# Kernel optimization log

Measured on AMD Instinct MI355X. Metric: run time of the kernel, lower is better.

Reference implementation:

```python
import jax, jax.numpy as jnp
import numpy as np

EPS = 1e-6

def layernorm2d(x, w, b):
    # x: [B,C,H,W]; normalize over channel dim per spatial location
    mu = jnp.mean(x, axis=1, keepdims=True)
    var = jnp.var(x, axis=1, keepdims=True)
    xn = (x - mu) / jnp.sqrt(var + EPS)
    return xn * w[None, :, None, None] + b[None, :, None, None]

def mish(x):
    return x * jnp.tanh(jax.nn.softplus(x))

def setup_inputs() -> dict:
    key = jax.random.key(0)
    ks = jax.random.split(key, 16)
    B, C, H, W, T = 16, 192, 96, 96, 512
    s = 0.02
    return {
        "t": jax.random.normal(ks[0], (B, T), jnp.float32),
        "x_l": jax.random.normal(ks[1], (B, C, H, W), jnp.float32),
        "x_r": jax.random.normal(ks[2], (B, C, H, W), jnp.float32),
        "ln_wl": jnp.ones((C,), jnp.float32),
        "ln_bl": jnp.zeros((C,), jnp.float32),
        "ln_wr": jnp.ones((C,), jnp.float32),
        "ln_br": jnp.zeros((C,), jnp.float32),
        "Wl1": jax.random.normal(ks[3], (C, C), jnp.float32) * s,
        "bl1": jnp.zeros((C,), jnp.float32),
        "Wr1": jax.random.normal(ks[4], (C, C), jnp.float32) * s,
        "br1": jnp.zeros((C,), jnp.float32),
        "Wl2": jax.random.normal(ks[5], (C, C), jnp.float32) * s,
        "bl2": jnp.zeros((C,), jnp.float32),
        "Wr2": jax.random.normal(ks[6], (C, C), jnp.float32) * s,
        "br2": jnp.zeros((C,), jnp.float32),
        "beta": jnp.zeros((C,), jnp.float32),
        "gamma": jnp.zeros((C,), jnp.float32),
        "Wt": jax.random.normal(ks[7], (C, T), jnp.float32) * s,
        "bt": jnp.zeros((C,), jnp.float32),
    }

def reference(t, x_l, x_r, ln_wl, ln_bl, ln_wr, ln_br,
              Wl1, bl1, Wr1, br1, Wl2, bl2, Wr2, br2,
              beta, gamma, Wt, bt):
    C = x_l.shape[1]
    scale = C ** (-0.5)
    # 1x1 convs as channel einsums; outputs in bhwc layout
    Q_l = jnp.einsum('bchw,oc->bhwo', layernorm2d(x_l, ln_wl, ln_bl), Wl1) + bl1  # [B,H,Wl,C]
    Q_r = jnp.einsum('bchw,oc->bhwo', layernorm2d(x_r, ln_wr, ln_br), Wr1) + br1  # [B,H,Wr,C]
    V_l = jnp.einsum('bchw,oc->bhwo', x_l, Wl2) + bl2
    V_r = jnp.einsum('bchw,oc->bhwo', x_r, Wr2) + br2
    att = jnp.einsum('bhxc,bhyc->bhxy', Q_l, Q_r) * scale  # [B,H,Wl,Wr]
    F_r2l = jnp.einsum('bhxy,bhyc->bhxc', jax.nn.softmax(att, axis=-1), V_r)
    F_l2r = jnp.einsum('bhxy,bhxc->bhyc', jax.nn.softmax(att, axis=2), V_l)
    temb = (mish(t) @ Wt.T + bt)[:, :, None, None]  # [B,C,1,1]
    out_l = x_l + jnp.transpose(F_r2l, (0, 3, 1, 2)) * beta[None, :, None, None] + temb
    out_r = x_r + jnp.transpose(F_l2r, (0, 3, 1, 2)) * gamma[None, :, None, None] + temb
    return (out_l, out_r)
```

## Files before the change

### kernel.cpp

```cpp
#include <hip/hip_runtime.h>
#include <hip/hip_bf16.h>


typedef __attribute__((ext_vector_type(8))) short bhalf8;
typedef __attribute__((ext_vector_type(4))) short bhalf4;
typedef __attribute__((ext_vector_type(4))) float f32x4;

#define DEVI static __device__ __forceinline__

constexpr int Cc   = 192;
constexpr int HWc  = 9216;
constexpr int CHW  = 192 * 9216;
constexpr int HALF_OUT = 16 * CHW;
constexpr int PPS  = 100;
constexpr int AS   = 100;

DEVI unsigned short f2bf(float f) {
  __hip_bfloat16 h = __float2bfloat16(f);
  return __builtin_bit_cast(unsigned short, h);
}
DEVI unsigned pk2bf(float a, float b) {
  return (unsigned)f2bf(a) | ((unsigned)f2bf(b) << 16);
}
DEVI float bf2f(unsigned short h) {
  unsigned u = (unsigned)h << 16;
  return __builtin_bit_cast(float, u);
}
DEVI float bf2f_s(short h) { return bf2f((unsigned short)h); }

__global__ void setup1(
    const float* __restrict__ t,
    const float* __restrict__ lnwl, const float* __restrict__ lnbl,
    const float* __restrict__ lnwr, const float* __restrict__ lnbr,
    const float* __restrict__ Wl1, const float* __restrict__ bl1,
    const float* __restrict__ Wr1, const float* __restrict__ br1,
    const float* __restrict__ Wl2, const float* __restrict__ Wr2,
    short* __restrict__ W1l_b, short* __restrict__ W1r_b,
    short* __restrict__ W2l_b, short* __restrict__ W2r_b,
    float* __restrict__ s1l, float* __restrict__ t1l,
    float* __restrict__ s1r, float* __restrict__ t1r,
    float* __restrict__ mt)
{
  const int blk = blockIdx.x, tid = threadIdx.x;
  if (blk < 576) {
    int id  = blk * 256 + tid;
    int m   = id / 36864;
    int rem = id - m * 36864;
    int c   = rem % 192;
    float v;
    short* dst;
    if (m == 0)      { v = lnwl[c] * Wl1[rem]; dst = W1l_b; }
    else if (m == 1) { v = lnwr[c] * Wr1[rem]; dst = W1r_b; }
    else if (m == 2) { v = Wl2[rem];           dst = W2l_b; }
    else             { v = Wr2[rem];           dst = W2r_b; }
    dst[rem] = (short)f2bf(v);
  } else if (blk == 576 || blk == 577) {
    if (tid < 192) {
      const float* Wm = (blk == 576) ? Wl1 : Wr1;
      const float* lw = (blk == 576) ? lnwl : lnwr;
      const float* lb = (blk == 576) ? lnbl : lnbr;
      const float* bb = (blk == 576) ? bl1 : br1;
      float s = 0.f, tb = 0.f;
      for (int c = 0; c < 192; ++c) {
        float wv = Wm[tid * 192 + c];
        s  += lw[c] * wv;
        tb += lb[c] * wv;
      }
      if (blk == 576) { s1l[tid] = s; t1l[tid] = tb + bb[tid]; }
      else            { s1r[tid] = s; t1r[tid] = tb + bb[tid]; }
    }
  } else {
    int id = (blk - 578) * 256 + tid;
    float v = t[id];
    float sp = (v > 20.f) ? v : log1pf(__expf(v));
    mt[id] = v * tanhf(sp);
  }
}

__global__ void setup2(const float* __restrict__ mt, const float* __restrict__ Wt,
                       const float* __restrict__ bt, float* __restrict__ temb)
{
  int id = blockIdx.x * 256 + threadIdx.x;
  int b = id / 192, o = id - b * 192;
  float s = 0.f;
  for (int k = 0; k < 512; ++k) s += mt[b * 512 + k] * Wt[o * 512 + k];
  temb[id] = s + bt[o];
}

struct SmemT {
  short xl[19200];
  short xr[19200];
  short q1[19200];
  short q2[19200];
  float misc[960];
};
static_assert(sizeof(SmemT) <= 163840, "LDS overflow");

__launch_bounds__(768, 3)
__global__ void scam_main(
    const float* __restrict__ x_l, const float* __restrict__ x_r,
    const float* __restrict__ bl2, const float* __restrict__ br2,
    const float* __restrict__ beta, const float* __restrict__ gamma,
    const short* __restrict__ W1l_b, const short* __restrict__ W1r_b,
    const short* __restrict__ W2l_b, const short* __restrict__ W2r_b,
    const float* __restrict__ s1l, const float* __restrict__ t1l,
    const float* __restrict__ s1r, const float* __restrict__ t1r,
    const float* __restrict__ temb,
    float* __restrict__ out)
{
  __shared__ SmemT sm;
  const int tid  = threadIdx.x;
  const int lane = tid & 63;
  const int wid  = tid >> 6;
  const int m16  = lane & 15;
  const int hb   = lane >> 4;
  const int kc8  = hb * 8;
  const int r4   = hb * 4;
  const int slice = blockIdx.x;
  const int bb_ = slice / 96;
  const int hh_ = slice - bb_ * 96;
  const int sliceBase = bb_ * CHW + hh_ * 96;
  const int o_wm = wid * 16 + m16;

  if (tid < 576) {
    int a = tid / 192, o = tid - a * 192;
    if (a == 0)      sm.misc[384 + o] = temb[bb_ * 192 + o];
    else if (a == 1) sm.misc[576 + o] = beta[o];
    else             sm.misc[768 + o] = gamma[o];
  }

  #pragma unroll
  for (int j = 0; j < 6; ++j) {
    int i4 = j * 768 + tid;
    int c  = i4 / 24;
    int w4 = i4 - c * 24;
    const float4 xl4 = *reinterpret_cast<const float4*>(x_l + sliceBase + c * HWc + w4 * 4);
    const float4 xr4 = *reinterpret_cast<const float4*>(x_r + sliceBase + c * HWc + w4 * 4);
    int sw = ((((c >> 3) ^ (w4 & 7)) << 3) | (c & 7));
    int base = w4 * 800 + sw;
    sm.xl[base      ] = (short)f2bf(xl4.x);
    sm.xl[base + 200] = (short)f2bf(xl4.y);
    sm.xl[base + 400] = (short)f2bf(xl4.z);
    sm.xl[base + 600] = (short)f2bf(xl4.w);
    sm.xr[base      ] = (short)f2bf(xr4.x);
    sm.xr[base + 200] = (short)f2bf(xr4.y);
    sm.xr[base + 400] = (short)f2bf(xr4.z);
    sm.xr[base + 600] = (short)f2bf(xr4.w);
  }
  __syncthreads();

  {
    int side = (tid >= 384) ? 1 : 0;
    int rest = tid - side * 384;
    int w = rest >> 2;
    int q = rest & 3;
    const short* Xb = side ? sm.xr : sm.xl;
    const int kxw = (w >> 2) & 7;
    float s0 = 0.f, s2 = 0.f;
    #pragma unroll
    for (int mc = 0; mc < 6; ++mc) {
      bhalf8 v = *reinterpret_cast<const bhalf8*>(Xb + w * 200 + (((q * 6 + mc) ^ kxw) << 3));
      #pragma unroll
      for (int e = 0; e < 8; ++e) { float f = bf2f_s(v[e]); s0 += f; s2 += f * f; }
    }
    s0 += __shfl_xor(s0, 1); s2 += __shfl_xor(s2, 1);
    s0 += __shfl_xor(s0, 2); s2 += __shfl_xor(s2, 2);
    if (q == 0) {
      float mu  = s0 * (1.f / 192.f);
      float var = s2 * (1.f / 192.f) - mu * mu;
      float rs  = rsqrtf(var + 1e-6f);
      sm.misc[side * 192 + w]      = mu;
      sm.misc[side * 192 + 96 + w] = rs;
    }
  }

  uint2 vRl[6], vRr[6];
  #pragma unroll
  for (int sd = 0; sd < 2; ++sd) {
    const short* Wb = sd ? W2r_b : W2l_b;
    const short* Xb = sd ? sm.xr : sm.xl;
    const float bv = (sd ? br2 : bl2)[o_wm];
    bhalf8 af[6];
    #pragma unroll
    for (int k = 0; k < 6; ++k)
      af[k] = *reinterpret_cast<const bhalf8*>(Wb + o_wm * 192 + k * 32 + kc8);
    #pragma unroll
    for (int xi = 0; xi < 6; ++xi) {
      const int row = xi * 16 + m16;
      const int kxr = (row >> 2) & 7;
      const short* Xr = Xb + row * 200;
      f32x4 acc = {0.f, 0.f, 0.f, 0.f};
      #pragma unroll
      for (int k = 0; k < 6; ++k) {
        bhalf8 bfr = *reinterpret_cast<const bhalf8*>(Xr + (((k * 4 + hb) ^ kxr) << 3));
        acc = __builtin_amdgcn_mfma_f32_16x16x32_bf16(bfr, af[k], acc, 0, 0, 0);
      }
      uint2 pv;
      pv.x = pk2bf(acc[0] + bv, acc[1] + bv);
      pv.y = pk2bf(acc[2] + bv, acc[3] + bv);
      if (sd) vRr[xi] = pv; else vRl[xi] = pv;
    }
  }

  f32x4 accQ[6];
  {
    bhalf8 bfq[6];
    #pragma unroll
    for (int k = 0; k < 6; ++k)
      bfq[k] = *reinterpret_cast<const bhalf8*>(W1l_b + o_wm * 192 + k * 32 + kc8);
    #pragma unroll
    for (int mi = 0; mi < 6; ++mi) {
      const int row = mi * 16 + m16;
      const int kxr = (row >> 2) & 7;
      const short* Xr = sm.xl + row * 200;
      f32x4 acc = {0.f, 0.f, 0.f, 0.f};
      #pragma unroll
      for (int k = 0; k < 6; ++k) {
        bhalf8 afr = *reinterpret_cast<const bhalf8*>(Xr + (((k * 4 + hb) ^ kxr) << 3));
        acc = __builtin_amdgcn_mfma_f32_16x16x32_bf16(bfq[k], afr, acc, 0, 0, 0);
      }
      accQ[mi] = acc;
    }
  }
  __syncthreads();
  {
    const int obase = wid * 16 + r4;
    const int oblk  = obase >> 3;
    const int osub  = (hb & 1) * 4;
    const float* muA = sm.misc;
    const float* rsA = sm.misc + 96;
    float s1v[4], t1v[4];
    #pragma unroll
    for (int j = 0; j < 4; ++j) { s1v[j] = s1l[obase + j]; t1v[j] = t1l[obase + j]; }
    #pragma unroll
    for (int mi = 0; mi < 6; ++mi) {
      const int x = mi * 16 + m16;
      const int kx = (x >> 2) & 7;
      float mu = muA[x], rs = rsA[x];
      float mrs = mu * rs;
      f32x4 acc = accQ[mi];
      uint2 pv;
      pv.x = pk2bf(rs * acc[0] - mrs * s1v[0] + t1v[0],
                   rs * acc[1] - mrs * s1v[1] + t1v[1]);
      pv.y = pk2bf(rs * acc[2] - mrs * s1v[2] + t1v[2],
                   rs * acc[3] - mrs * s1v[3] + t1v[3]);
      *reinterpret_cast<uint2*>(sm.q1 + x * 200 + (((oblk ^ kx) << 3) | osub)) = pv;
    }
  }
  {
    bhalf8 bfq[6];
    #pragma unroll
    for (int k = 0; k < 6; ++k)
      bfq[k] = *reinterpret_cast<const bhalf8*>(W1r_b + o_wm * 192 + k * 32 + kc8);
    #pragma unroll
    for (int mi = 0; mi < 6; ++mi) {
      const int row = mi * 16 + m16;
      const int kxr = (row >> 2) & 7;
      const short* Xr = sm.xr + row * 200;
      f32x4 acc = {0.f, 0.f, 0.f, 0.f};
      #pragma unroll
      for (int k = 0; k < 6; ++k) {
        bhalf8 afr = *reinterpret_cast<const bhalf8*>(Xr + (((k * 4 + hb) ^ kxr) << 3));
        acc = __builtin_amdgcn_mfma_f32_16x16x32_bf16(bfq[k], afr, acc, 0, 0, 0);
      }
      accQ[mi] = acc;
    }
  }
  {
    const int obase = wid * 16 + r4;
    const int oblk  = obase >> 3;
    const int osub  = (hb & 1) * 4;
    const float* muA = sm.misc + 192;
    const float* rsA = sm.misc + 288;
    float s1v[4], t1v[4];
    #pragma unroll
    for (int j = 0; j < 4; ++j) { s1v[j] = s1r[obase + j]; t1v[j] = t1r[obase + j]; }
    #pragma unroll
    for (int mi = 0; mi < 6; ++mi) {
      const int x = mi * 16 + m16;
      const int kx = (x >> 2) & 7;
      float mu = muA[x], rs = rsA[x];
      float mrs = mu * rs;
      f32x4 acc = accQ[mi];
      uint2 pv;
      pv.x = pk2bf(rs * acc[0] - mrs * s1v[0] + t1v[0],
                   rs * acc[1] - mrs * s1v[1] + t1v[1]);
      pv.y = pk2bf(rs * acc[2] - mrs * s1v[2] + t1v[2],
                   rs * acc[3] - mrs * s1v[3] + t1v[3]);
      *reinterpret_cast<uint2*>(sm.q2 + x * 200 + (((oblk ^ kx) << 3) | osub)) = pv;
    }
  }
  __syncthreads();

  {
    const int mi = wid >> 1;
    const int yb = (wid & 1) * 3;
    const int arow = mi * 16 + m16;
    const int kxa = (arow >> 2) & 7;
    bhalf8 afa[6];
    #pragma unroll
    for (int k = 0; k < 6; ++k)
      afa[k] = *reinterpret_cast<const bhalf8*>(sm.q1 + arow * 200 + (((k * 4 + hb) ^ kxa) << 3));
    f32x4 accA[3];
    #pragma unroll
    for (int yt = 0; yt < 3; ++yt) {
      const int brow = (yb + yt) * 16 + m16;
      const int kxb = (brow >> 2) & 7;
      const short* Br = sm.q2 + brow * 200;
      f32x4 acc = {0.f, 0.f, 0.f, 0.f};
      #pragma unroll
      for (int k = 0; k < 6; ++k) {
        bhalf8 bfy = *reinterpret_cast<const bhalf8*>(Br + (((k * 4 + hb) ^ kxb) << 3));
        acc = __builtin_amdgcn_mfma_f32_16x16x32_bf16(afa[k], bfy, acc, 0, 0, 0);
      }
      accA[yt] = acc;
    }
    __syncthreads();
    float* attf = reinterpret_cast<float*>(sm.q1);
    const float scale = 0.07216878364870323f;
    #pragma unroll
    for (int yt = 0; yt < 3; ++yt) {
      #pragma unroll
      for (int j = 0; j < 4; ++j) {
        int x = mi * 16 + r4 + j;
        int y = (yb + yt) * 16 + m16;
        attf[x * AS + (y ^ (x & 31))] = accA[yt][j] * scale;
      }
    }
  }
  __syncthreads();

  {
    const float* attf = reinterpret_cast<const float*>(sm.q1);
    short* Pr = sm.q2;
    short* Pc = sm.q2 + 96 * PPS;
    const int r = tid >> 3;
    const int p = tid & 7;
    {
      float av[12];
      #pragma unroll
      for (int k = 0; k < 12; ++k)
        av[k] = attf[r * AS + ((p * 12 + k) ^ (r & 31))];
      float mx = av[0];
      #pragma unroll
      for (int k = 1; k < 12; ++k) mx = fmaxf(mx, av[k]);
      mx = fmaxf(mx, __shfl_xor(mx, 1));
      mx = fmaxf(mx, __shfl_xor(mx, 2));
      mx = fmaxf(mx, __shfl_xor(mx, 4));
      float s = 0.f;
      #pragma unroll
      for (int k = 0; k < 12; ++k) { av[k] = __expf(av[k] - mx); s += av[k]; }
      s += __shfl_xor(s, 1); s += __shfl_xor(s, 2); s += __shfl_xor(s, 4);
      float inv = 1.f / s;
      #pragma unroll
      for (int k = 0; k < 12; k += 2) {
        *reinterpret_cast<unsigned*>(Pr + r * PPS + p * 12 + k) =
            pk2bf(av[k] * inv, av[k + 1] * inv);
      }
    }
    {
      float av[12];
      #pragma unroll
      for (int k = 0; k < 12; ++k) {
        int x = p * 12 + k;
        av[k] = attf[x * AS + (r ^ (x & 31))];
      }
      float mx = av[0];
      #pragma unroll
      for (int k = 1; k < 12; ++k) mx = fmaxf(mx, av[k]);
      mx = fmaxf(mx, __shfl_xor(mx, 1));
      mx = fmaxf(mx, __shfl_xor(mx, 2));
      mx = fmaxf(mx, __shfl_xor(mx, 4));
      float s = 0.f;
      #pragma unroll
      for (int k = 0; k < 12; ++k) { av[k] = __expf(av[k] - mx); s += av[k]; }
      s += __shfl_xor(s, 1); s += __shfl_xor(s, 2); s += __shfl_xor(s, 4);
      float inv = 1.f / s;
      #pragma unroll
      for (int k = 0; k < 12; k += 2) {
        *reinterpret_cast<unsigned*>(Pc + r * PPS + p * 12 + k) =
            pk2bf(av[k] * inv, av[k + 1] * inv);
      }
    }
  }
  __syncthreads();

  f32x4 accL[6];
  {
    const short* Pr = sm.q2;
    const short* Pc = sm.q2 + 96 * PPS;
    const int cblk = (wid * 16 + r4) >> 3;
    const int csub = (hb & 1) * 4;
    #pragma unroll
    for (int xt = 0; xt < 6; ++xt) {
      const int x = xt * 16 + m16;
      f32x4 acc = {0.f, 0.f, 0.f, 0.f};
      #pragma unroll
      for (int kt = 0; kt < 6; ++kt) {
        bhalf4 a = __builtin_bit_cast(bhalf4, vRr[kt]);
        bhalf4 b = *reinterpret_cast<const bhalf4*>(Pr + x * PPS + kt * 16 + hb * 4);
        acc = __builtin_amdgcn_mfma_f32_16x16x16bf16_1k(a, b, acc, 0, 0, 0);
      }
      const int kx = (x >> 2) & 7;
      const int off = x * 200 + (((cblk ^ kx) << 3) | csub);
      uint2 pf;
      pf.x = pk2bf(acc[0], acc[1]);
      pf.y = pk2bf(acc[2], acc[3]);
      *reinterpret_cast<uint2*>(sm.q1 + off) = pf;
    }
    #pragma unroll
    for (int yt = 0; yt < 6; ++yt) {
      const int y = yt * 16 + m16;
      f32x4 acc = {0.f, 0.f, 0.f, 0.f};
      #pragma unroll
      for (int kt = 0; kt < 6; ++kt) {
        bhalf4 a = __builtin_bit_cast(bhalf4, vRl[kt]);
        bhalf4 b = *reinterpret_cast<const bhalf4*>(Pc + y * PPS + kt * 16 + hb * 4);
        acc = __builtin_amdgcn_mfma_f32_16x16x16bf16_1k(a, b, acc, 0, 0, 0);
      }
      accL[yt] = acc;
    }
  }
  __syncthreads();
  {
    const int cblk = (wid * 16 + r4) >> 3;
    const int csub = (hb & 1) * 4;
    #pragma unroll
    for (int yt = 0; yt < 6; ++yt) {
      const int y = yt * 16 + m16;
      const int kx = (y >> 2) & 7;
      const int off = y * 200 + (((cblk ^ kx) << 3) | csub);
      uint2 pg;
      pg.x = pk2bf(accL[yt][0], accL[yt][1]);
      pg.y = pk2bf(accL[yt][2], accL[yt][3]);
      *reinterpret_cast<uint2*>(sm.q2 + off) = pg;
    }
  }
  __syncthreads();

  #pragma unroll
  for (int sd = 0; sd < 2; ++sd) {
    float* og = out + (sd ? HALF_OUT : 0);
    const short* Fb = sd ? sm.q2 : sm.q1;
    const short* Xb = sd ? sm.xr : sm.xl;
    const float* coef = sm.misc + (sd ? 768 : 576);
    #pragma unroll
    for (int j = 0; j < 6; ++j) {
      int i4 = j * 768 + tid;
      int c  = i4 / 24;
      int w4 = i4 - c * 24;
      float cf = coef[c];
      float tv = sm.misc[384 + c];
      int sw = ((((c >> 3) ^ (w4 & 7)) << 3) | (c & 7));
      int fb = w4 * 800 + sw;
      float4 ov;
      ov.x = bf2f_s(Xb[fb      ]) + bf2f_s(Fb[fb      ]) * cf + tv;
      ov.y = bf2f_s(Xb[fb + 200]) + bf2f_s(Fb[fb + 200]) * cf + tv;
      ov.z = bf2f_s(Xb[fb + 400]) + bf2f_s(Fb[fb + 400]) * cf + tv;
      ov.w = bf2f_s(Xb[fb + 600]) + bf2f_s(Fb[fb + 600]) * cf + tv;
      *reinterpret_cast<float4*>(og + sliceBase + c * HWc + w4 * 4) = ov;
    }
  }
}

extern "C" void kernel_launch(void* const* d_in, const int* in_sizes, int n_in,
                              void* d_out, int out_size, void* d_ws, size_t ws_size,
                              hipStream_t stream)
{
  const float* t    = (const float*)d_in[0];
  const float* x_l  = (const float*)d_in[1];
  const float* x_r  = (const float*)d_in[2];
  const float* lnwl = (const float*)d_in[3];
  const float* lnbl = (const float*)d_in[4];
  const float* lnwr = (const float*)d_in[5];
  const float* lnbr = (const float*)d_in[6];
  const float* Wl1  = (const float*)d_in[7];
  const float* bl1  = (const float*)d_in[8];
  const float* Wr1  = (const float*)d_in[9];
  const float* br1  = (const float*)d_in[10];
  const float* Wl2  = (const float*)d_in[11];
  const float* bl2  = (const float*)d_in[12];
  const float* Wr2  = (const float*)d_in[13];
  const float* br2  = (const float*)d_in[14];
  const float* beta = (const float*)d_in[15];
  const float* gamma= (const float*)d_in[16];
  const float* Wt   = (const float*)d_in[17];
  const float* bt   = (const float*)d_in[18];
  float* out = (float*)d_out;

  char* ws = (char*)d_ws;
  short* W1l_b = (short*)ws;
  short* W1r_b = W1l_b + 36864;
  short* W2l_b = W1r_b + 36864;
  short* W2r_b = W2l_b + 36864;
  float* fws  = (float*)(ws + 4 * 73728);
  float* s1l  = fws;
  float* t1l  = fws + 192;
  float* s1r  = fws + 384;
  float* t1r  = fws + 576;
  float* temb = fws + 768;
  float* mt   = fws + 3840;

  setup1<<<610, 256, 0, stream>>>(t, lnwl, lnbl, lnwr, lnbr, Wl1, bl1, Wr1, br1,
                                  Wl2, Wr2, W1l_b, W1r_b, W2l_b, W2r_b,
                                  s1l, t1l, s1r, t1r, mt);
  setup2<<<12, 256, 0, stream>>>(mt, Wt, bt, temb);
  scam_main<<<1536, 768, 0, stream>>>(x_l, x_r, bl2, br2, beta, gamma,
                                      W1l_b, W1r_b, W2l_b, W2r_b,
                                      s1l, t1l, s1r, t1r, temb, out);
}
```

Baseline: 254.3 us.

## Process six rows per block with software-prefetched next-slice loads

Each workgroup now handles six consecutive H rows in a loop instead of one, with the grid shrunk from 1536 to 256 blocks. The next row's x_l and x_r are loaded into registers during the softmax and PV stages, then written to shared memory once the current row's buffers are free, so global latency overlaps with compute. The residual add now rereads fp32 x from global memory instead of the bf16 copy in shared memory, which changes precision slightly and adds traffic. With only 256 blocks on a 256-CU part there is one block per CU and less latency hiding across blocks, and the registers needed for prefetch may raise register pressure.

After: 978.4 us. +284.8%, slower.

```diff
diff --git a/kernel.cpp b/kernel.cpp
--- a/kernel.cpp
+++ b/kernel.cpp
@@ -116,11 +116,12 @@
   const int hb   = lane >> 4;
   const int kc8  = hb * 8;
   const int r4   = hb * 4;
-  const int slice = blockIdx.x;
-  const int bb_ = slice / 96;
-  const int hh_ = slice - bb_ * 96;
-  const int sliceBase = bb_ * CHW + hh_ * 96;
+  const int wg   = blockIdx.x;
+  const int bb_  = wg >> 4;
+  const int hh0  = 6 * (wg & 15);
+  const int baseB = bb_ * CHW;
   const int o_wm = wid * 16 + m16;
+
 
   if (tid < 576) {
     int a = tid / 192, o = tid - a * 192;
@@ -128,338 +129,398 @@
     else if (a == 1) sm.misc[576 + o] = beta[o];
     else             sm.misc[768 + o] = gamma[o];
   }
-
-  #pragma unroll
-  for (int j = 0; j < 6; ++j) {
-    int i4 = j * 768 + tid;
-    int c  = i4 / 24;
-    int w4 = i4 - c * 24;
-    const float4 xl4 = *reinterpret_cast<const float4*>(x_l + sliceBase + c * HWc + w4 * 4);
-    const float4 xr4 = *reinterpret_cast<const float4*>(x_r + sliceBase + c * HWc + w4 * 4);
-    int sw = ((((c >> 3) ^ (w4 & 7)) << 3) | (c & 7));
-    int base = w4 * 800 + sw;
-    sm.xl[base      ] = (short)f2bf(xl4.x);
-    sm.xl[base + 200] = (short)f2bf(xl4.y);
-    sm.xl[base + 400] = (short)f2bf(xl4.z);
-    sm.xl[base + 600] = (short)f2bf(xl4.w);
-    sm.xr[base      ] = (short)f2bf(xr4.x);
-    sm.xr[base + 200] = (short)f2bf(xr4.y);
-    sm.xr[base + 400] = (short)f2bf(xr4.z);
-    sm.xr[base + 600] = (short)f2bf(xr4.w);
-  }
-  __syncthreads();
-
   {
-    int side = (tid >= 384) ? 1 : 0;
-    int rest = tid - side * 384;
-    int w = rest >> 2;
-    int q = rest & 3;
-    const short* Xb = side ? sm.xr : sm.xl;
-    const int kxw = (w >> 2) & 7;
-    float s0 = 0.f, s2 = 0.f;
-    #pragma unroll
-    for (int mc = 0; mc < 6; ++mc) {
-      bhalf8 v = *reinterpret_cast<const bhalf8*>(Xb + w * 200 + (((q * 6 + mc) ^ kxw) << 3));
-      #pragma unroll
-      for (int e = 0; e < 8; ++e) { float f = bf2f_s(v[e]); s0 += f; s2 += f * f; }
-    }
-    s0 += __shfl_xor(s0, 1); s2 += __shfl_xor(s2, 1);
-    s0 += __shfl_xor(s0, 2); s2 += __shfl_xor(s2, 2);
-    if (q == 0) {
-      float mu  = s0 * (1.f / 192.f);
-      float var = s2 * (1.f / 192.f) - mu * mu;
-      float rs  = rsqrtf(var + 1e-6f);
-      sm.misc[side * 192 + w]      = mu;
-      sm.misc[side * 192 + 96 + w] = rs;
-    }
-  }
-
-  uint2 vRl[6], vRr[6];
-  #pragma unroll
-  for (int sd = 0; sd < 2; ++sd) {
-    const short* Wb = sd ? W2r_b : W2l_b;
-    const short* Xb = sd ? sm.xr : sm.xl;
-    const float bv = (sd ? br2 : bl2)[o_wm];
-    bhalf8 af[6];
-    #pragma unroll
-    for (int k = 0; k < 6; ++k)
-      af[k] = *reinterpret_cast<const bhalf8*>(Wb + o_wm * 192 + k * 32 + kc8);
-    #pragma unroll
-    for (int xi = 0; xi < 6; ++xi) {
-      const int row = xi * 16 + m16;
-      const int kxr = (row >> 2) & 7;
-      const short* Xr = Xb + row * 200;
-      f32x4 acc = {0.f, 0.f, 0.f, 0.f};
-      #pragma unroll
-      for (int k = 0; k < 6; ++k) {
-        bhalf8 bfr = *reinterpret_cast<const bhalf8*>(Xr + (((k * 4 + hb) ^ kxr) << 3));
-        acc = __builtin_amdgcn_mfma_f32_16x16x32_bf16(bfr, af[k], acc, 0, 0, 0);
-      }
-      uint2 pv;
-      pv.x = pk2bf(acc[0] + bv, acc[1] + bv);
-      pv.y = pk2bf(acc[2] + bv, acc[3] + bv);
-      if (sd) vRr[xi] = pv; else vRl[xi] = pv;
-    }
-  }
-
-  f32x4 accQ[6];
-  {
-    bhalf8 bfq[6];
-    #pragma unroll
-    for (int k = 0; k < 6; ++k)
-      bfq[k] = *reinterpret_cast<const bhalf8*>(W1l_b + o_wm * 192 + k * 32 + kc8);
-    #pragma unroll
-    for (int mi = 0; mi < 6; ++mi) {
-      const int row = mi * 16 + m16;
-      const int kxr = (row >> 2) & 7;
-      const short* Xr = sm.xl + row * 200;
-      f32x4 acc = {0.f, 0.f, 0.f, 0.f};
-      #pragma unroll
-      for (int k = 0; k < 6; ++k) {
-        bhalf8 afr = *reinterpret_cast<const bhalf8*>(Xr + (((k * 4 + hb) ^ kxr) << 3));
-        acc = __builtin_amdgcn_mfma_f32_16x16x32_bf16(bfq[k], afr, acc, 0, 0, 0);
-      }
-      accQ[mi] = acc;
-    }
-  }
-  __syncthreads();
-  {
-    const int obase = wid * 16 + r4;
-    const int oblk  = obase >> 3;
-    const int osub  = (hb & 1) * 4;
-    const float* muA = sm.misc;
-    const float* rsA = sm.misc + 96;
-    float s1v[4], t1v[4];
-    #pragma unroll
-    for (int j = 0; j < 4; ++j) { s1v[j] = s1l[obase + j]; t1v[j] = t1l[obase + j]; }
-    #pragma unroll
-    for (int mi = 0; mi < 6; ++mi) {
-      const int x = mi * 16 + m16;
-      const int kx = (x >> 2) & 7;
-      float mu = muA[x], rs = rsA[x];
-      float mrs = mu * rs;
-      f32x4 acc = accQ[mi];
-      uint2 pv;
-      pv.x = pk2bf(rs * acc[0] - mrs * s1v[0] + t1v[0],
-                   rs * acc[1] - mrs * s1v[1] + t1v[1]);
-      pv.y = pk2bf(rs * acc[2] - mrs * s1v[2] + t1v[2],
-                   rs * acc[3] - mrs * s1v[3] + t1v[3]);
-      *reinterpret_cast<uint2*>(sm.q1 + x * 200 + (((oblk ^ kx) << 3) | osub)) = pv;
-    }
-  }
-  {
-    bhalf8 bfq[6];
-    #pragma unroll
-    for (int k = 0; k < 6; ++k)
-      bfq[k] = *reinterpret_cast<const bhalf8*>(W1r_b + o_wm * 192 + k * 32 + kc8);
-    #pragma unroll
-    for (int mi = 0; mi < 6; ++mi) {
-      const int row = mi * 16 + m16;
-      const int kxr = (row >> 2) & 7;
-      const short* Xr = sm.xr + row * 200;
-      f32x4 acc = {0.f, 0.f, 0.f, 0.f};
-      #pragma unroll
-      for (int k = 0; k < 6; ++k) {
-        bhalf8 afr = *reinterpret_cast<const bhalf8*>(Xr + (((k * 4 + hb) ^ kxr) << 3));
-        acc = __builtin_amdgcn_mfma_f32_16x16x32_bf16(bfq[k], afr, acc, 0, 0, 0);
-      }
-      accQ[mi] = acc;
-    }
-  }
-  {
-    const int obase = wid * 16 + r4;
-    const int oblk  = obase >> 3;
-    const int osub  = (hb & 1) * 4;
-    const float* muA = sm.misc + 192;
-    const float* rsA = sm.misc + 288;
-    float s1v[4], t1v[4];
-    #pragma unroll
-    for (int j = 0; j < 4; ++j) { s1v[j] = s1r[obase + j]; t1v[j] = t1r[obase + j]; }
-    #pragma unroll
-    for (int mi = 0; mi < 6; ++mi) {
-      const int x = mi * 16 + m16;
-      const int kx = (x >> 2) & 7;
-      float mu = muA[x], rs = rsA[x];
-      float mrs = mu * rs;
-      f32x4 acc = accQ[mi];
-      uint2 pv;
-      pv.x = pk2bf(rs * acc[0] - mrs * s1v[0] + t1v[0],
-                   rs * acc[1] - mrs * s1v[1] + t1v[1]);
-      pv.y = pk2bf(rs * acc[2] - mrs * s1v[2] + t1v[2],
-                   rs * acc[3] - mrs * s1v[3] + t1v[3]);
-      *reinterpret_cast<uint2*>(sm.q2 + x * 200 + (((oblk ^ kx) << 3) | osub)) = pv;
-    }
-  }
-  __syncthreads();
-
-  {
-    const int mi = wid >> 1;
-    const int yb = (wid & 1) * 3;
-    const int arow = mi * 16 + m16;
-    const int kxa = (arow >> 2) & 7;
-    bhalf8 afa[6];
-    #pragma unroll
-    for (int k = 0; k < 6; ++k)
-      afa[k] = *reinterpret_cast<const bhalf8*>(sm.q1 + arow * 200 + (((k * 4 + hb) ^ kxa) << 3));
-    f32x4 accA[3];
-    #pragma unroll
-    for (int yt = 0; yt < 3; ++yt) {
-      const int brow = (yb + yt) * 16 + m16;
-      const int kxb = (brow >> 2) & 7;
-      const short* Br = sm.q2 + brow * 200;
-      f32x4 acc = {0.f, 0.f, 0.f, 0.f};
-      #pragma unroll
-      for (int k = 0; k < 6; ++k) {
-        bhalf8 bfy = *reinterpret_cast<const bhalf8*>(Br + (((k * 4 + hb) ^ kxb) << 3));
-        acc = __builtin_amdgcn_mfma_f32_16x16x32_bf16(afa[k], bfy, acc, 0, 0, 0);
-      }
-      accA[yt] = acc;
-    }
-    __syncthreads();
-    float* attf = reinterpret_cast<float*>(sm.q1);
-    const float scale = 0.07216878364870323f;
-    #pragma unroll
-    for (int yt = 0; yt < 3; ++yt) {
-      #pragma unroll
-      for (int j = 0; j < 4; ++j) {
-        int x = mi * 16 + r4 + j;
-        int y = (yb + yt) * 16 + m16;
-        attf[x * AS + (y ^ (x & 31))] = accA[yt][j] * scale;
-      }
-    }
-  }
-  __syncthreads();
-
-  {
-    const float* attf = reinterpret_cast<const float*>(sm.q1);
-    short* Pr = sm.q2;
-    short* Pc = sm.q2 + 96 * PPS;
-    const int r = tid >> 3;
-    const int p = tid & 7;
-    {
-      float av[12];
-      #pragma unroll
-      for (int k = 0; k < 12; ++k)
-        av[k] = attf[r * AS + ((p * 12 + k) ^ (r & 31))];
-      float mx = av[0];
-      #pragma unroll
-      for (int k = 1; k < 12; ++k) mx = fmaxf(mx, av[k]);
-      mx = fmaxf(mx, __shfl_xor(mx, 1));
-      mx = fmaxf(mx, __shfl_xor(mx, 2));
-      mx = fmaxf(mx, __shfl_xor(mx, 4));
-      float s = 0.f;
-      #pragma unroll
-      for (int k = 0; k < 12; ++k) { av[k] = __expf(av[k] - mx); s += av[k]; }
-      s += __shfl_xor(s, 1); s += __shfl_xor(s, 2); s += __shfl_xor(s, 4);
-      float inv = 1.f / s;
-      #pragma unroll
-      for (int k = 0; k < 12; k += 2) {
-        *reinterpret_cast<unsigned*>(Pr + r * PPS + p * 12 + k) =
-            pk2bf(av[k] * inv, av[k + 1] * inv);
-      }
-    }
-    {
-      float av[12];
-      #pragma unroll
-      for (int k = 0; k < 12; ++k) {
-        int x = p * 12 + k;
-        av[k] = attf[x * AS + (r ^ (x & 31))];
-      }
-      float mx = av[0];
-      #pragma unroll
-      for (int k = 1; k < 12; ++k) mx = fmaxf(mx, av[k]);
-      mx = fmaxf(mx, __shfl_xor(mx, 1));
-      mx = fmaxf(mx, __shfl_xor(mx, 2));
-      mx = fmaxf(mx, __shfl_xor(mx, 4));
-      float s = 0.f;
-      #pragma unroll
-      for (int k = 0; k < 12; ++k) { av[k] = __expf(av[k] - mx); s += av[k]; }
-      s += __shfl_xor(s, 1); s += __shfl_xor(s, 2); s += __shfl_xor(s, 4);
-      float inv = 1.f / s;
-      #pragma unroll
-      for (int k = 0; k < 12; k += 2) {
-        *reinterpret_cast<unsigned*>(Pc + r * PPS + p * 12 + k) =
-            pk2bf(av[k] * inv, av[k + 1] * inv);
-      }
-    }
-  }
-  __syncthreads();
-
-  f32x4 accL[6];
-  {
-    const short* Pr = sm.q2;
-    const short* Pc = sm.q2 + 96 * PPS;
-    const int cblk = (wid * 16 + r4) >> 3;
-    const int csub = (hb & 1) * 4;
-    #pragma unroll
-    for (int xt = 0; xt < 6; ++xt) {
-      const int x = xt * 16 + m16;
-      f32x4 acc = {0.f, 0.f, 0.f, 0.f};
-      #pragma unroll
-      for (int kt = 0; kt < 6; ++kt) {
-        bhalf4 a = __builtin_bit_cast(bhalf4, vRr[kt]);
-        bhalf4 b = *reinterpret_cast<const bhalf4*>(Pr + x * PPS + kt * 16 + hb * 4);
-        acc = __builtin_amdgcn_mfma_f32_16x16x16bf16_1k(a, b, acc, 0, 0, 0);
-      }
-      const int kx = (x >> 2) & 7;
-      const int off = x * 200 + (((cblk ^ kx) << 3) | csub);
-      uint2 pf;
-      pf.x = pk2bf(acc[0], acc[1]);
-      pf.y = pk2bf(acc[2], acc[3]);
-      *reinterpret_cast<uint2*>(sm.q1 + off) = pf;
-    }
-    #pragma unroll
-    for (int yt = 0; yt < 6; ++yt) {
-      const int y = yt * 16 + m16;
-      f32x4 acc = {0.f, 0.f, 0.f, 0.f};
-      #pragma unroll
-      for (int kt = 0; kt < 6; ++kt) {
-        bhalf4 a = __builtin_bit_cast(bhalf4, vRl[kt]);
-        bhalf4 b = *reinterpret_cast<const bhalf4*>(Pc + y * PPS + kt * 16 + hb * 4);
-        acc = __builtin_amdgcn_mfma_f32_16x16x16bf16_1k(a, b, acc, 0, 0, 0);
-      }
-      accL[yt] = acc;
-    }
-  }
-  __syncthreads();
-  {
-    const int cblk = (wid * 16 + r4) >> 3;
-    const int csub = (hb & 1) * 4;
-    #pragma unroll
-    for (int yt = 0; yt < 6; ++yt) {
-      const int y = yt * 16 + m16;
-      const int kx = (y >> 2) & 7;
-      const int off = y * 200 + (((cblk ^ kx) << 3) | csub);
-      uint2 pg;
-      pg.x = pk2bf(accL[yt][0], accL[yt][1]);
-      pg.y = pk2bf(accL[yt][2], accL[yt][3]);
-      *reinterpret_cast<uint2*>(sm.q2 + off) = pg;
-    }
-  }
-  __syncthreads();
-
-  #pragma unroll
-  for (int sd = 0; sd < 2; ++sd) {
-    float* og = out + (sd ? HALF_OUT : 0);
-    const short* Fb = sd ? sm.q2 : sm.q1;
-    const short* Xb = sd ? sm.xr : sm.xl;
-    const float* coef = sm.misc + (sd ? 768 : 576);
+    const int sb = baseB + hh0 * 96;
     #pragma unroll
     for (int j = 0; j < 6; ++j) {
       int i4 = j * 768 + tid;
       int c  = i4 / 24;
       int w4 = i4 - c * 24;
-      float cf = coef[c];
-      float tv = sm.misc[384 + c];
+      const float4 xl4 = *reinterpret_cast<const float4*>(x_l + sb + c * HWc + w4 * 4);
+      const float4 xr4 = *reinterpret_cast<const float4*>(x_r + sb + c * HWc + w4 * 4);
       int sw = ((((c >> 3) ^ (w4 & 7)) << 3) | (c & 7));
-      int fb = w4 * 800 + sw;
-      float4 ov;
-      ov.x = bf2f_s(Xb[fb      ]) + bf2f_s(Fb[fb      ]) * cf + tv;
-      ov.y = bf2f_s(Xb[fb + 200]) + bf2f_s(Fb[fb + 200]) * cf + tv;
-      ov.z = bf2f_s(Xb[fb + 400]) + bf2f_s(Fb[fb + 400]) * cf + tv;
-      ov.w = bf2f_s(Xb[fb + 600]) + bf2f_s(Fb[fb + 600]) * cf + tv;
-      *reinterpret_cast<float4*>(og + sliceBase + c * HWc + w4 * 4) = ov;
-    }
+      int base = w4 * 800 + sw;
+      sm.xl[base      ] = (short)f2bf(xl4.x);
+      sm.xl[base + 200] = (short)f2bf(xl4.y);
+      sm.xl[base + 400] = (short)f2bf(xl4.z);
+      sm.xl[base + 600] = (short)f2bf(xl4.w);
+      sm.xr[base      ] = (short)f2bf(xr4.x);
+      sm.xr[base + 200] = (short)f2bf(xr4.y);
+      sm.xr[base + 400] = (short)f2bf(xr4.z);
+      sm.xr[base + 600] = (short)f2bf(xr4.w);
+    }
+  }
+  __syncthreads();
+
+  #pragma unroll 1
+  for (int it = 0; it < 6; ++it) {
+    const int sliceBase = baseB + (hh0 + it) * 96;
+    float4 xsl[6], xsr[6];
+
+    {
+      int side = (tid >= 384) ? 1 : 0;
+      int rest = tid - side * 384;
+      int w = rest >> 2;
+      int q = rest & 3;
+      const short* Xb = side ? sm.xr : sm.xl;
+      const int kxw = (w >> 2) & 7;
+      float s0 = 0.f, s2 = 0.f;
+      #pragma unroll
+      for (int mc = 0; mc < 6; ++mc) {
+        bhalf8 v = *reinterpret_cast<const bhalf8*>(Xb + w * 200 + (((q * 6 + mc) ^ kxw) << 3));
+        #pragma unroll
+        for (int e = 0; e < 8; ++e) { float f = bf2f_s(v[e]); s0 += f; s2 += f * f; }
+      }
+      s0 += __shfl_xor(s0, 1); s2 += __shfl_xor(s2, 1);
+      s0 += __shfl_xor(s0, 2); s2 += __shfl_xor(s2, 2);
+      if (q == 0) {
+        float mu  = s0 * (1.f / 192.f);
+        float var = s2 * (1.f / 192.f) - mu * mu;
+        float rs  = rsqrtf(var + 1e-6f);
+        sm.misc[side * 192 + w]      = mu;
+        sm.misc[side * 192 + 96 + w] = rs;
+      }
+    }
+
+    uint2 vRl[6], vRr[6];
+    #pragma unroll
+    for (int sd = 0; sd < 2; ++sd) {
+      const short* Wb = sd ? W2r_b : W2l_b;
+      const short* Xb = sd ? sm.xr : sm.xl;
+      const float bv = (sd ? br2 : bl2)[o_wm];
+      bhalf8 af[6];
+      #pragma unroll
+      for (int k = 0; k < 6; ++k)
+        af[k] = *reinterpret_cast<const bhalf8*>(Wb + o_wm * 192 + k * 32 + kc8);
+      #pragma unroll
+      for (int xi = 0; xi < 6; ++xi) {
+        const int row = xi * 16 + m16;
+        const int kxr = (row >> 2) & 7;
+        const short* Xr = Xb + row * 200;
+        f32x4 acc = {0.f, 0.f, 0.f, 0.f};
+        #pragma unroll
+        for (int k = 0; k < 6; ++k) {
+          bhalf8 bfr = *reinterpret_cast<const bhalf8*>(Xr + (((k * 4 + hb) ^ kxr) << 3));
+          acc = __builtin_amdgcn_mfma_f32_16x16x32_bf16(bfr, af[k], acc, 0, 0, 0);
+        }
+        uint2 pv;
+        pv.x = pk2bf(acc[0] + bv, acc[1] + bv);
+        pv.y = pk2bf(acc[2] + bv, acc[3] + bv);
+        if (sd) vRr[xi] = pv; else vRl[xi] = pv;
+      }
+    }
+
+    f32x4 accQ[6];
+    {
+      bhalf8 bfq[6];
+      #pragma unroll
+      for (int k = 0; k < 6; ++k)
+        bfq[k] = *reinterpret_cast<const bhalf8*>(W1l_b + o_wm * 192 + k * 32 + kc8);
+      #pragma unroll
+      for (int mi = 0; mi < 6; ++mi) {
+        const int row = mi * 16 + m16;
+        const int kxr = (row >> 2) & 7;
+        const short* Xr = sm.xl + row * 200;
+        f32x4 acc = {0.f, 0.f, 0.f, 0.f};
+        #pragma unroll
+        for (int k = 0; k < 6; ++k) {
+          bhalf8 afr = *reinterpret_cast<const bhalf8*>(Xr + (((k * 4 + hb) ^ kxr) << 3));
+          acc = __builtin_amdgcn_mfma_f32_16x16x32_bf16(bfq[k], afr, acc, 0, 0, 0);
+        }
+        accQ[mi] = acc;
+      }
+    }
+    __syncthreads();
+    {
+      const int obase = wid * 16 + r4;
+      const int oblk  = obase >> 3;
+      const int osub  = (hb & 1) * 4;
+      const float* muA = sm.misc;
+      const float* rsA = sm.misc + 96;
+      float s1v[4], t1v[4];
+      #pragma unroll
+      for (int j = 0; j < 4; ++j) { s1v[j] = s1l[obase + j]; t1v[j] = t1l[obase + j]; }
+      #pragma unroll
+      for (int mi = 0; mi < 6; ++mi) {
+        const int x = mi * 16 + m16;
+        const int kx = (x >> 2) & 7;
+        float mu = muA[x], rs = rsA[x];
+        float mrs = mu * rs;
+        f32x4 acc = accQ[mi];
+        uint2 pv;
+        pv.x = pk2bf(rs * acc[0] - mrs * s1v[0] + t1v[0],
+                     rs * acc[1] - mrs * s1v[1] + t1v[1]);
+        pv.y = pk2bf(rs * acc[2] - mrs * s1v[2] + t1v[2],
+                     rs * acc[3] - mrs * s1v[3] + t1v[3]);
+        *reinterpret_cast<uint2*>(sm.q1 + x * 200 + (((oblk ^ kx) << 3) | osub)) = pv;
+      }
+    }
+    {
+      bhalf8 bfq[6];
+      #pragma unroll
+      for (int k = 0; k < 6; ++k)
+        bfq[k] = *reinterpret_cast<const bhalf8*>(W1r_b + o_wm * 192 + k * 32 + kc8);
+      #pragma unroll
+      for (int mi = 0; mi < 6; ++mi) {
+        const int row = mi * 16 + m16;
+        const int kxr = (row >> 2) & 7;
+        const short* Xr = sm.xr + row * 200;
+        f32x4 acc = {0.f, 0.f, 0.f, 0.f};
+        #pragma unroll
+        for (int k = 0; k < 6; ++k) {
+          bhalf8 afr = *reinterpret_cast<const bhalf8*>(Xr + (((k * 4 + hb) ^ kxr) << 3));
+          acc = __builtin_amdgcn_mfma_f32_16x16x32_bf16(bfq[k], afr, acc, 0, 0, 0);
+        }
+        accQ[mi] = acc;
+      }
+    }
+    {
+      const int obase = wid * 16 + r4;
+      const int oblk  = obase >> 3;
+      const int osub  = (hb & 1) * 4;
+      const float* muA = sm.misc + 192;
+      const float* rsA = sm.misc + 288;
+      float s1v[4], t1v[4];
+      #pragma unroll
+      for (int j = 0; j < 4; ++j) { s1v[j] = s1r[obase + j]; t1v[j] = t1r[obase + j]; }
+      #pragma unroll
+      for (int mi = 0; mi < 6; ++mi) {
+        const int x = mi * 16 + m16;
+        const int kx = (x >> 2) & 7;
+        float mu = muA[x], rs = rsA[x];
+        float mrs = mu * rs;
+        f32x4 acc = accQ[mi];
+        uint2 pv;
+        pv.x = pk2bf(rs * acc[0] - mrs * s1v[0] + t1v[0],
+                     rs * acc[1] - mrs * s1v[1] + t1v[1]);
+        pv.y = pk2bf(rs * acc[2] - mrs * s1v[2] + t1v[2],
+                     rs * acc[3] - mrs * s1v[3] + t1v[3]);
+        *reinterpret_cast<uint2*>(sm.q2 + x * 200 + (((oblk ^ kx) << 3) | osub)) = pv;
+      }
+    }
+    __syncthreads();
+
+    {
+      const int mi = wid >> 1;
+      const int yb = (wid & 1) * 3;
+      const int arow = mi * 16 + m16;
+      const int kxa = (arow >> 2) & 7;
+      bhalf8 afa[6];
+      #pragma unroll
+      for (int k = 0; k < 6; ++k)
+        afa[k] = *reinterpret_cast<const bhalf8*>(sm.q1 + arow * 200 + (((k * 4 + hb) ^ kxa) << 3));
+      f32x4 accA[3];
+      #pragma unroll
+      for (int yt = 0; yt < 3; ++yt) {
+        const int brow = (yb + yt) * 16 + m16;
+        const int kxb = (brow >> 2) & 7;
+        const short* Br = sm.q2 + brow * 200;
+        f32x4 acc = {0.f, 0.f, 0.f, 0.f};
+        #pragma unroll
+        for (int k = 0; k < 6; ++k) {
+          bhalf8 bfy = *reinterpret_cast<const bhalf8*>(Br + (((k * 4 + hb) ^ kxb) << 3));
+          acc = __builtin_amdgcn_mfma_f32_16x16x32_bf16(afa[k], bfy, acc, 0, 0, 0);
+        }
+        accA[yt] = acc;
+      }
+      __syncthreads();
+      float* attf = reinterpret_cast<float*>(sm.q1);
+      const float scale = 0.07216878364870323f;
+      #pragma unroll
+      for (int yt = 0; yt < 3; ++yt) {
+        #pragma unroll
+        for (int j = 0; j < 4; ++j) {
+          int x = mi * 16 + r4 + j;
+          int y = (yb + yt) * 16 + m16;
+          attf[x * AS + (y ^ (x & 31))] = accA[yt][j] * scale;
+        }
+      }
+    }
+    __syncthreads();
+
+    if (it < 5) {
+      const int sbn = sliceBase + 96;
+      #pragma unroll
+      for (int j = 0; j < 6; ++j) {
+        int i4 = j * 768 + tid;
+        int c  = i4 / 24;
+        int w4 = i4 - c * 24;
+        xsl[j] = *reinterpret_cast<const float4*>(x_l + sbn + c * HWc + w4 * 4);
+      }
+    }
+
+    {
+      const float* attf = reinterpret_cast<const float*>(sm.q1);
+      short* Pr = sm.q2;
+      short* Pc = sm.q2 + 96 * PPS;
+      const int r = tid >> 3;
+      const int p = tid & 7;
+      {
+        float av[12];
+        #pragma unroll
+        for (int k = 0; k < 12; ++k)
+          av[k] = attf[r * AS + ((p * 12 + k) ^ (r & 31))];
+        float mx = av[0];
+        #pragma unroll
+        for (int k = 1; k < 12; ++k) mx = fmaxf(mx, av[k]);
+        mx = fmaxf(mx, __shfl_xor(mx, 1));
+        mx = fmaxf(mx, __shfl_xor(mx, 2));
+        mx = fmaxf(mx, __shfl_xor(mx, 4));
+        float s = 0.f;
+        #pragma unroll
+        for (int k = 0; k < 12; ++k) { av[k] = __expf(av[k] - mx); s += av[k]; }
+        s += __shfl_xor(s, 1); s += __shfl_xor(s, 2); s += __shfl_xor(s, 4);
+        float inv = 1.f / s;
+        #pragma unroll
+        for (int k = 0; k < 12; k += 2) {
+          *reinterpret_cast<unsigned*>(Pr + r * PPS + p * 12 + k) =
+              pk2bf(av[k] * inv, av[k + 1] * inv);
+        }
+      }
+      {
+        float av[12];
+        #pragma unroll
+        for (int k = 0; k < 12; ++k) {
+          int x = p * 12 + k;
+          av[k] = attf[x * AS + (r ^ (x & 31))];
+        }
+        float mx = av[0];
+        #pragma unroll
+        for (int k = 1; k < 12; ++k) mx = fmaxf(mx, av[k]);
+        mx = fmaxf(mx, __shfl_xor(mx, 1));
+        mx = fmaxf(mx, __shfl_xor(mx, 2));
+        mx = fmaxf(mx, __shfl_xor(mx, 4));
+        float s = 0.f;
+        #pragma unroll
+        for (int k = 0; k < 12; ++k) { av[k] = __expf(av[k] - mx); s += av[k]; }
+        s += __shfl_xor(s, 1); s += __shfl_xor(s, 2); s += __shfl_xor(s, 4);
+        float inv = 1.f / s;
+        #pragma unroll
+        for (int k = 0; k < 12; k += 2) {
+          *reinterpret_cast<unsigned*>(Pc + r * PPS + p * 12 + k) =
+              pk2bf(av[k] * inv, av[k + 1] * inv);
+        }
+      }
+    }
+    __syncthreads();
+
+    if (it < 5) {
+      #pragma unroll
+      for (int j = 0; j < 6; ++j) {
+        int i4 = j * 768 + tid;
+        int c  = i4 / 24;
+        int w4 = i4 - c * 24;
+        int sw = ((((c >> 3) ^ (w4 & 7)) << 3) | (c & 7));
+        int base = w4 * 800 + sw;
+        sm.xl[base      ] = (short)f2bf(xsl[j].x);
+        sm.xl[base + 200] = (short)f2bf(xsl[j].y);
+        sm.xl[base + 400] = (short)f2bf(xsl[j].z);
+        sm.xl[base + 600] = (short)f2bf(xsl[j].w);
+      }
+      const int sbn = sliceBase + 96;
+      #pragma unroll
+      for (int j = 0; j < 6; ++j) {
+        int i4 = j * 768 + tid;
+        int c  = i4 / 24;
+        int w4 = i4 - c * 24;
+        xsr[j] = *reinterpret_cast<const float4*>(x_r + sbn + c * HWc + w4 * 4);
+      }
+    }
+
+    f32x4 accL[6];
+    {
+      const short* Pr = sm.q2;
+      const short* Pc = sm.q2 + 96 * PPS;
+      const int cblk = (wid * 16 + r4) >> 3;
+      const int csub = (hb & 1) * 4;
+      #pragma unroll
+      for (int xt = 0; xt < 6; ++xt) {
+        const int x = xt * 16 + m16;
+        f32x4 acc = {0.f, 0.f, 0.f, 0.f};
+        #pragma unroll
+        for (int kt = 0; kt < 6; ++kt) {
+          bhalf4 a = __builtin_bit_cast(bhalf4, vRr[kt]);
+          bhalf4 b = *reinterpret_cast<const bhalf4*>(Pr + x * PPS + kt * 16 + hb * 4);
+          acc = __builtin_amdgcn_mfma_f32_16x16x16bf16_1k(a, b, acc, 0, 0, 0);
+        }
+        const int kx = (x >> 2) & 7;
+        const int off = x * 200 + (((cblk ^ kx) << 3) | csub);
+        uint2 pf;
+        pf.x = pk2bf(acc[0], acc[1]);
+        pf.y = pk2bf(acc[2], acc[3]);
+        *reinterpret_cast<uint2*>(sm.q1 + off) = pf;
+      }
+      #pragma unroll
+      for (int yt = 0; yt < 6; ++yt) {
+        const int y = yt * 16 + m16;
+        f32x4 acc = {0.f, 0.f, 0.f, 0.f};
+        #pragma unroll
+        for (int kt = 0; kt < 6; ++kt) {
+          bhalf4 a = __builtin_bit_cast(bhalf4, vRl[kt]);
+          bhalf4 b = *reinterpret_cast<const bhalf4*>(Pc + y * PPS + kt * 16 + hb * 4);
+          acc = __builtin_amdgcn_mfma_f32_16x16x16bf16_1k(a, b, acc, 0, 0, 0);
+        }
+        accL[yt] = acc;
+      }
+    }
+    __syncthreads();
+
+    if (it < 5) {
+      #pragma unroll
+      for (int j = 0; j < 6; ++j) {
+        int i4 = j * 768 + tid;
+        int c  = i4 / 24;
+        int w4 = i4 - c * 24;
+        int sw = ((((c >> 3) ^ (w4 & 7)) << 3) | (c & 7));
+        int base = w4 * 800 + sw;
+        sm.xr[base      ] = (short)f2bf(xsr[j].x);
+        sm.xr[base + 200] = (short)f2bf(xsr[j].y);
+        sm.xr[base + 400] = (short)f2bf(xsr[j].z);
+        sm.xr[base + 600] = (short)f2bf(xsr[j].w);
+      }
+    }
+
+    {
+      const int cblk = (wid * 16 + r4) >> 3;
+      const int csub = (hb & 1) * 4;
+      #pragma unroll
+      for (int yt = 0; yt < 6; ++yt) {
+        const int y = yt * 16 + m16;
+        const int kx = (y >> 2) & 7;
+        const int off = y * 200 + (((cblk ^ kx) << 3) | csub);
+        uint2 pg;
+        pg.x = pk2bf(accL[yt][0], accL[yt][1]);
+        pg.y = pk2bf(accL[yt][2], accL[yt][3]);
+        *reinterpret_cast<uint2*>(sm.q2 + off) = pg;
+      }
+    }
+    __syncthreads();
+
+    #pragma unroll
+    for (int sd = 0; sd < 2; ++sd) {
+      const float* xg = sd ? x_r : x_l;
+      float* og = out + (sd ? HALF_OUT : 0);
+      const short* Fb = sd ? sm.q2 : sm.q1;
+      const float* coef = sm.misc + (sd ? 768 : 576);
+      #pragma unroll
+      for (int j = 0; j < 6; ++j) {
+        int i4 = j * 768 + tid;
+        int c  = i4 / 24;
+        int w4 = i4 - c * 24;
+        const float4 xv = *reinterpret_cast<const float4*>(xg + sliceBase + c * HWc + w4 * 4);
+        float cf = coef[c];
+        float tv = sm.misc[384 + c];
+        int sw = ((((c >> 3) ^ (w4 & 7)) << 3) | (c & 7));
+        int fb = w4 * 800 + sw;
+        float4 ov;
+        ov.x = xv.x + bf2f_s(Fb[fb      ]) * cf + tv;
+        ov.y = xv.y + bf2f_s(Fb[fb + 200]) * cf + tv;
+        ov.z = xv.z + bf2f_s(Fb[fb + 400]) * cf + tv;
+        ov.w = xv.w + bf2f_s(Fb[fb + 600]) * cf + tv;
+        *reinterpret_cast<float4*>(og + sliceBase + c * HWc + w4 * 4) = ov;
+      }
+    }
+    __syncthreads();
   }
 }
 
@@ -505,7 +566,7 @@
                                   Wl2, Wr2, W1l_b, W1r_b, W2l_b, W2r_b,
                                   s1l, t1l, s1r, t1r, mt);
   setup2<<<12, 256, 0, stream>>>(mt, Wt, bt, temb);
-  scam_main<<<1536, 768, 0, stream>>>(x_l, x_r, bl2, br2, beta, gamma,
-                                      W1l_b, W1r_b, W2l_b, W2r_b,
-                                      s1l, t1l, s1r, t1r, temb, out);
-}
+  scam_main<<<256, 768, 0, stream>>>(x_l, x_r, bl2, br2, beta, gamma,
+                                     W1l_b, W1r_b, W2l_b, W2r_b,
+                                     s1l, t1l, s1r, t1r, temb, out);
+}
```
